# Kernel tuning notes

Measured on AMD Instinct MI355X. Metric: run time of the kernel, lower is better.

## Reference

```python
import jax, jax.numpy as jnp
import numpy as np

V, I, H, O = 10000, 64, 128, 128   # vocab, in_size, hidden_size, out_size
T, L = 4096, 64                    # num traces, max trace length


def setup_inputs() -> dict:
    key = jax.random.key(0)
    ks = jax.random.split(key, 18)
    s = 0.05
    n = jax.random.normal
    inp = {
        "emb":   n(ks[0], (V, I)) * s,
        # torch nn.LSTM layer 0: weight_ih [4H, I], weight_hh [4H, H], biases [4H]
        "W_ih1": n(ks[1], (4 * H, I)) * s,
        "W_hh1": n(ks[2], (4 * H, H)) * s,
        "b_ih1": n(ks[3], (4 * H,)) * s,
        "b_hh1": n(ks[4], (4 * H,)) * s,
        # layer 1
        "W_ih2": n(ks[5], (4 * H, H)) * s,
        "W_hh2": n(ks[6], (4 * H, H)) * s,
        "b_ih2": n(ks[7], (4 * H,)) * s,
        "b_hh2": n(ks[8], (4 * H,)) * s,
        # attention MLP: hidden -> 64 -> 1
        "Wp1":   n(ks[9], (64, H)) * s,
        "bp1":   n(ks[10], (64,)) * s,
        "Wp2":   n(ks[11], (1, 64)) * s,
        "bp2":   n(ks[12], (1,)) * s,
        # out_layer
        "W_out": n(ks[13], (O, H)) * s,
        "b_out": n(ks[14], (O,)) * s,
        "traces": jax.random.randint(ks[15], (T, L), 0, V, dtype=jnp.int32),
        "lengths": jnp.maximum(jax.random.randint(ks[16], (T,), 1, L + 1, dtype=jnp.int32), 1),
    }
    return inp


def _lstm_step(x, W_ih, b_ih, b_hh):
    # Single LSTM timestep from zero state (h0=c0=0), per token.
    # Gate order in torch: i, f, g, o. f*c0 = 0 so f is computed-but-unused.
    g = x @ W_ih.T + b_ih + b_hh                      # [T, L, 4H]
    i, f, c_hat, o = jnp.split(g, 4, axis=-1)
    c = jax.nn.sigmoid(i) * jnp.tanh(c_hat)
    return jax.nn.sigmoid(o) * jnp.tanh(c)            # [T, L, H]


def reference(emb, W_ih1, W_hh1, b_ih1, b_hh1, W_ih2, W_hh2, b_ih2, b_hh2,
              Wp1, bp1, Wp2, bp2, W_out, b_out, traces, lengths):
    x = emb[traces]                                   # [T, L, I]
    h1 = _lstm_step(x, W_ih1, b_ih1, b_hh1)           # [T, L, H]
    h2 = _lstm_step(h1, W_ih2, b_ih2, b_hh2)          # [T, L, H]  (hidden_out)
    # SelfAttention over positions within each trace
    energy = (jax.nn.relu(h2 @ Wp1.T + bp1) @ Wp2.T + bp2)[..., 0]  # [T, L]
    mask = jnp.arange(L)[None, :] < lengths[:, None]  # [T, L] valid positions
    energy = jnp.where(mask, energy, -1e30)
    w = jax.nn.softmax(energy, axis=1)                # [T, L]
    trace_emb = jnp.einsum("tlh,tl->th", h2, w)      # [T, H]
    final = trace_emb.sum(axis=0)                     # [H]  (sum over traces)
    return final @ W_out.T + b_out                    # [O]
```

## Files before the change

### kernel.cpp

```cpp
#include <hip/hip_runtime.h>
#include <stdint.h>

typedef unsigned short u16;
typedef __attribute__((ext_vector_type(8))) short short8;
typedef __attribute__((ext_vector_type(4))) float f32x4;
typedef __attribute__((ext_vector_type(4))) unsigned int u32x4;

#define NTRACE 4096
#define TLEN   64
#define ISZ    64
#define HSZ    128
#define NBIN   64
#define VSZ    10000

#define LOG2E     1.44269504088896f
#define TWOLOG2E  2.88539008177793f

__device__ __forceinline__ float bflo(uint32_t u) {
  union { uint32_t i; float f; } v; v.i = u << 16; return v.f;
}
__device__ __forceinline__ float bfhi(uint32_t u) {
  union { uint32_t i; float f; } v; v.i = u & 0xffff0000u; return v.f;
}
__device__ __forceinline__ u16 f2bf(float f) {
  union { float f; uint32_t i; } v; v.f = f;
  uint32_t r = v.i + 0x7fffu + ((v.i >> 16) & 1u);
  return (u16)(r >> 16);
}
__device__ __forceinline__ float fexp2(float x) {
  float r;
  asm("v_exp_f32 %0, %1" : "=v"(r) : "v"(x));
  return r;
}
__device__ __forceinline__ float gate2(float gB, float gE) {
  float E = fexp2(gE);
  float B = fexp2(gB);
  return (E - 1.0f) * __builtin_amdgcn_rcpf((E + 1.0f) * (1.0f + B));
}
__device__ __forceinline__ short8 mk8(uint32_t a, uint32_t b, uint32_t c, uint32_t d) {
  union { short8 s; uint32_t u[4]; } z;
  z.u[0] = a; z.u[1] = b; z.u[2] = c; z.u[3] = d; return z.s;
}
union S8 { short8 s; u16 h[8]; };
__device__ __forceinline__ int perm128(int rr) {
  return ((rr >> 4) & 3) * 32 + ((rr >> 2) & 3) * 8 + ((rr >> 6) & 1) * 4 + (rr & 3);
}

__global__ __launch_bounds__(256) void k_prep(
    const float* __restrict__ W1, const float* __restrict__ W2,
    const float* __restrict__ Wp1,
    const float* __restrict__ b_ih1, const float* __restrict__ b_hh1,
    const float* __restrict__ b_ih2, const float* __restrict__ b_hh2,
    u16* __restrict__ w1c, u16* __restrict__ w2c, u16* __restrict__ wp1b,
    float* __restrict__ bs1, float* __restrict__ bs2,
    float* __restrict__ bins)
{
  const int i = blockIdx.x * 256 + threadIdx.x;
  if (i < 3072) {
    const int r    = i >> 3;
    const int G3   = r >> 7;
    const int rawG = (G3 == 0) ? 0 : ((G3 == 1) ? 2 : 3);
    const int src  = rawG * 128 + perm128(r & 127);
    const float s  = (G3 == 1) ? TWOLOG2E : -LOG2E;
    const int c16  = (i & 7) * 8;
    const float* wsrc = W1 + (size_t)src * ISZ + c16;
    uint32_t pkk[4];
#pragma unroll
    for (int k = 0; k < 4; ++k)
      pkk[k] = (uint32_t)f2bf(wsrc[2 * k] * s) |
               ((uint32_t)f2bf(wsrc[2 * k + 1] * s) << 16);
    *(u32x4*)&w1c[r * 64 + (c16 ^ ((r & 7) << 3))] = *(u32x4*)pkk;
  }
  if (i < 6144) {
    const int r    = i >> 4;
    const int G3   = r >> 7;
    const int rawG = (G3 == 0) ? 0 : ((G3 == 1) ? 2 : 3);
    const int src  = rawG * 128 + perm128(r & 127);
    const float s  = (G3 == 1) ? TWOLOG2E : -LOG2E;
    const int c16  = (i & 15) * 8;
    const float* wsrc = W2 + (size_t)src * HSZ + c16;
    uint32_t pkk[4];
#pragma unroll
    for (int k = 0; k < 4; ++k)
      pkk[k] = (uint32_t)f2bf(wsrc[2 * k] * s) |
               ((uint32_t)f2bf(wsrc[2 * k + 1] * s) << 16);
    *(u32x4*)&w2c[r * 128 + (c16 ^ ((r & 15) << 3))] = *(u32x4*)pkk;
  }
  if (i < 64 * 128) wp1b[i] = f2bf(Wp1[i]);
  if (i < 512) {
    const int G = i >> 7, rr = i & 127;
    const float s = (G == 2) ? TWOLOG2E : -LOG2E;
    const int src = G * 128 + perm128(rr);
    bs1[i] = (b_ih1[src] + b_hh1[src]) * s;
    bs2[i] = (b_ih2[src] + b_hh2[src]) * s;
  }
  if (i < NBIN * HSZ) bins[i] = 0.f;
}

__global__ __launch_bounds__(512) void k_vocab(
    const float* __restrict__ emb,
    const u16* __restrict__ w1c, const u16* __restrict__ w2c,
    const float* __restrict__ bs1, const float* __restrict__ bs2,
    const u16* __restrict__ wp1b,
    const float* __restrict__ bp1v, const float* __restrict__ wp2v,
    float* __restrict__ Et, u16* __restrict__ H2t)
{
  __shared__ __align__(16) u16 w1s[384 * 64];
  __shared__ __align__(16) u16 w2s[384 * 128];
  const int tid = threadIdx.x;

  for (int i = tid; i < 3072; i += 512)
    ((u32x4*)w1s)[i] = ((const u32x4*)w1c)[i];
  for (int i = tid; i < 6144; i += 512)
    ((u32x4*)w2s)[i] = ((const u32x4*)w2c)[i];
  __syncthreads();

  const int lane = tid & 63;
  const int col  = lane & 15;
  const int q    = lane >> 4;
  const int sw1  = (col & 7) << 3;
  const int sw2  = col << 3;
  const int id   = (blockIdx.x * 8 + (tid >> 6)) * 16 + col;
  const int idc  = (id < VSZ) ? id : 0;
  const f32x4 z = {0.f, 0.f, 0.f, 0.f};

  short8 xf[2];
  {
    const float* xr = emb + (size_t)idc * ISZ + q * 8;
#pragma unroll
    for (int ks = 0; ks < 2; ++ks) {
      S8 v;
#pragma unroll
      for (int k = 0; k < 8; ++k) v.h[k] = f2bf(xr[ks * 32 + k]);
      xf[ks] = v.s;
    }
  }

  uint32_t pk[8][2];
#pragma unroll
  for (int mt = 0; mt < 8; ++mt) {
    f32x4 aI = z, aC = z, aO = z;
#pragma unroll
    for (int ks = 0; ks < 2; ++ks) {
      const int off = ((ks * 32 + q * 8) ^ sw1);
      short8 fI = *(const short8*)&w1s[(mt * 16 + col) * ISZ + off];
      short8 fC = *(const short8*)&w1s[(128 + mt * 16 + col) * ISZ + off];
      short8 fO = *(const short8*)&w1s[(256 + mt * 16 + col) * ISZ + off];
      aI = __builtin_amdgcn_mfma_f32_16x16x32_bf16(fI, xf[ks], aI, 0, 0, 0);
      aC = __builtin_amdgcn_mfma_f32_16x16x32_bf16(fC, xf[ks], aC, 0, 0, 0);
      aO = __builtin_amdgcn_mfma_f32_16x16x32_bf16(fO, xf[ks], aO, 0, 0, 0);
    }
    u16 hv[4];
#pragma unroll
    for (int r = 0; r < 4; ++r) {
      const int h = mt * 16 + q * 4 + r;
      float c = gate2(aI[r] + bs1[h], aC[r] + bs1[256 + h]);
      hv[r] = f2bf(gate2(aO[r] + bs1[384 + h], TWOLOG2E * c));
    }
    pk[mt][0] = (uint32_t)hv[0] | ((uint32_t)hv[1] << 16);
    pk[mt][1] = (uint32_t)hv[2] | ((uint32_t)hv[3] << 16);
  }

  short8 hf[4];
#pragma unroll
  for (int ks = 0; ks < 4; ++ks)
    hf[ks] = mk8(pk[ks][0], pk[ks][1], pk[ks + 4][0], pk[ks + 4][1]);

  uint32_t pk2[8][2];
#pragma unroll
  for (int mt = 0; mt < 8; ++mt) {
    f32x4 aI = z, aC = z, aO = z;
#pragma unroll
    for (int ks = 0; ks < 4; ++ks) {
      const int off = ((ks * 32 + q * 8) ^ sw2);
      short8 fI = *(const short8*)&w2s[(mt * 16 + col) * HSZ + off];
      short8 fC = *(const short8*)&w2s[(128 + mt * 16 + col) * HSZ + off];
      short8 fO = *(const short8*)&w2s[(256 + mt * 16 + col) * HSZ + off];
      aI = __builtin_amdgcn_mfma_f32_16x16x32_bf16(fI, hf[ks], aI, 0, 0, 0);
      aC = __builtin_amdgcn_mfma_f32_16x16x32_bf16(fC, hf[ks], aC, 0, 0, 0);
      aO = __builtin_amdgcn_mfma_f32_16x16x32_bf16(fO, hf[ks], aO, 0, 0, 0);
    }
    u16 hv[4];
#pragma unroll
    for (int r = 0; r < 4; ++r) {
      const int h = mt * 16 + q * 4 + r;
      float c = gate2(aI[r] + bs2[h], aC[r] + bs2[256 + h]);
      hv[r] = f2bf(gate2(aO[r] + bs2[384 + h], TWOLOG2E * c));
    }
    pk2[mt][0] = (uint32_t)hv[0] | ((uint32_t)hv[1] << 16);
    pk2[mt][1] = (uint32_t)hv[2] | ((uint32_t)hv[3] << 16);
  }

  short8 hf2[4];
#pragma unroll
  for (int ks = 0; ks < 4; ++ks)
    hf2[ks] = mk8(pk2[ks][0], pk2[ks][1], pk2[ks + 4][0], pk2[ks + 4][1]);

  float ep = 0.f;
#pragma unroll
  for (int mt = 0; mt < 4; ++mt) {
    f32x4 acc = z;
#pragma unroll
    for (int ks = 0; ks < 4; ++ks) {
      short8 fA = *(const short8*)(wp1b + (size_t)(mt * 16 + col) * HSZ + ks * 32 + q * 8);
      acc = __builtin_amdgcn_mfma_f32_16x16x32_bf16(fA, hf2[ks], acc, 0, 0, 0);
    }
#pragma unroll
    for (int r = 0; r < 4; ++r) {
      const int hp = mt * 16 + q * 4 + r;
      ep += fmaxf(acc[r] + bp1v[hp], 0.f) * wp2v[hp];
    }
  }
  ep += __shfl_xor(ep, 16);
  ep += __shfl_xor(ep, 32);

  if (id < VSZ) {
    if (q == 0) Et[id] = ep;
#pragma unroll
    for (int ks = 0; ks < 4; ++ks)
      *(short8*)&H2t[(size_t)id * HSZ + ks * 32 + q * 8] = hf2[ks];
  }
}

__global__ __launch_bounds__(256) void k_attn(
    const float* __restrict__ Et, const u16* __restrict__ H2t,
    const int* __restrict__ traces, const int* __restrict__ lengths,
    float* __restrict__ bins)
{
  const int wv   = threadIdx.x >> 6;
  const int lane = threadIdx.x & 63;
  const int t    = blockIdx.x * 4 + wv;
  const int len  = lengths[t];
  const int tok  = traces[t * TLEN + lane];
  const bool valid = lane < len;

  float e = valid ? Et[tok] : -3.0e38f;
  float m = e;
#pragma unroll
  for (int off = 1; off < 64; off <<= 1) m = fmaxf(m, __shfl_xor(m, off));
  float w = valid ? __expf(e - m) : 0.f;
  float s = w;
#pragma unroll
  for (int off = 1; off < 64; off <<= 1) s += __shfl_xor(s, off);
  const float wl = w * __builtin_amdgcn_rcpf(s);

  const int hc = lane * 2;
  float a0 = 0.f, a1 = 0.f;
  for (int l = 0; l < len; ++l) {
    const float wb = __shfl(wl, l);
    const int   tb = __shfl(tok, l);
    const uint32_t hv = *(const uint32_t*)&H2t[(size_t)tb * HSZ + hc];
    a0 += wb * bflo(hv);
    a1 += wb * bfhi(hv);
  }
  float* bin = bins + (size_t)(t & (NBIN - 1)) * HSZ;
  atomicAdd(&bin[hc], a0);
  atomicAdd(&bin[hc + 1], a1);
}

__global__ __launch_bounds__(128) void k_out(
    const float* __restrict__ bins, const float* __restrict__ W_out,
    const float* __restrict__ b_out, float* __restrict__ out)
{
  const int o = threadIdx.x;
  __shared__ float fs[HSZ];
  float s = 0.f;
#pragma unroll 4
  for (int b = 0; b < NBIN; ++b) s += bins[b * HSZ + o];
  fs[o] = s;
  __syncthreads();
  float acc = b_out[o];
  const float* wr = W_out + (size_t)o * HSZ;
#pragma unroll
  for (int h = 0; h < HSZ; ++h) acc += wr[h] * fs[h];
  out[o] = acc;
}

extern "C" void kernel_launch(void* const* d_in, const int* in_sizes, int n_in,
                              void* d_out, int out_size, void* d_ws, size_t ws_size,
                              hipStream_t stream)
{
  const float* emb   = (const float*)d_in[0];
  const float* W_ih1 = (const float*)d_in[1];
  const float* b_ih1 = (const float*)d_in[3];
  const float* b_hh1 = (const float*)d_in[4];
  const float* W_ih2 = (const float*)d_in[5];
  const float* b_ih2 = (const float*)d_in[7];
  const float* b_hh2 = (const float*)d_in[8];
  const float* Wp1   = (const float*)d_in[9];
  const float* bp1   = (const float*)d_in[10];
  const float* Wp2   = (const float*)d_in[11];
  const float* bp2   = (const float*)d_in[12];
  const float* W_out = (const float*)d_in[13];
  const float* b_out = (const float*)d_in[14];
  const int* traces  = (const int*)d_in[15];
  const int* lengths = (const int*)d_in[16];
  (void)bp2;

  char* ws = (char*)d_ws;
  float* Et   = (float*)(ws);
  u16*   H2t  = (u16*)(ws + 40960);
  float* bins = (float*)(ws + 2662400);
  u16*   w1c  = (u16*)(ws + 2695168);
  u16*   w2c  = (u16*)(ws + 2744320);
  u16*   wp1b = (u16*)(ws + 2842624);
  float* bs1  = (float*)(ws + 2859008);
  float* bs2  = (float*)(ws + 2861056);

  k_prep<<<32, 256, 0, stream>>>(W_ih1, W_ih2, Wp1, b_ih1, b_hh1,
                                 b_ih2, b_hh2, w1c, w2c, wp1b,
                                 bs1, bs2, bins);
  k_vocab<<<80, 512, 0, stream>>>(emb, w1c, w2c, bs1, bs2, wp1b,
                                  bp1, Wp2, Et, H2t);
  k_attn<<<NTRACE / 4, 256, 0, stream>>>(Et, H2t, traces, lengths, bins);
  k_out<<<1, 128, 0, stream>>>(bins, W_out, b_out, (float*)d_out);
}
```

Before: 138.3 us.

## Fuse weight prep into vocab kernel and output GEMV into attention kernel

Each of the 80 vocab blocks now converts the fp32 LSTM weights and biases to bf16 directly into shared memory, and converts Wp1 inline, so the separate prep kernel is gone. The output projection is folded into the attention kernel: an atomic counter picks the last block, which sums the bins and runs the output GEMV. This cuts the launch count from four to two, removing launch gaps and a workspace round trip. In exchange every vocab block repeats the fp32-to-bf16 conversion, and the attention kernel gains a threadfence, an atomic counter and atomic reads of the bins.

Result: slower. 152.6 us (+10.3%).

```diff
diff --git a/kernel.cpp b/kernel.cpp
--- a/kernel.cpp
+++ b/kernel.cpp
@@ -12,6 +12,7 @@
 #define HSZ    128
 #define NBIN   64
 #define VSZ    10000
+#define NATT   (NTRACE / 4)
 
 #define LOG2E     1.44269504088896f
 #define TWOLOG2E  2.88539008177793f
@@ -46,17 +47,29 @@
   return ((rr >> 4) & 3) * 32 + ((rr >> 2) & 3) * 8 + ((rr >> 6) & 1) * 4 + (rr & 3);
 }
 
-__global__ __launch_bounds__(256) void k_prep(
+__global__ __launch_bounds__(512) void k_vocab(
+    const float* __restrict__ emb,
     const float* __restrict__ W1, const float* __restrict__ W2,
-    const float* __restrict__ Wp1,
     const float* __restrict__ b_ih1, const float* __restrict__ b_hh1,
     const float* __restrict__ b_ih2, const float* __restrict__ b_hh2,
-    u16* __restrict__ w1c, u16* __restrict__ w2c, u16* __restrict__ wp1b,
-    float* __restrict__ bs1, float* __restrict__ bs2,
-    float* __restrict__ bins)
+    const float* __restrict__ Wp1,
+    const float* __restrict__ bp1v, const float* __restrict__ wp2v,
+    float* __restrict__ Et, u16* __restrict__ H2t,
+    float* __restrict__ bins, unsigned* __restrict__ ctr)
 {
-  const int i = blockIdx.x * 256 + threadIdx.x;
-  if (i < 3072) {
+  __shared__ __align__(16) u16 w1s[384 * 64];
+  __shared__ __align__(16) u16 w2s[384 * 128];
+  __shared__ float bsh1[512];
+  __shared__ float bsh2[512];
+  const int tid = threadIdx.x;
+
+  {
+    const int bz = blockIdx.x * 512 + tid;
+    if (bz < NBIN * HSZ) bins[bz] = 0.f;
+    if (blockIdx.x == 0 && tid == 0) *ctr = 0u;
+  }
+
+  for (int i = tid; i < 3072; i += 512) {
     const int r    = i >> 3;
     const int G3   = r >> 7;
     const int rawG = (G3 == 0) ? 0 : ((G3 == 1) ? 2 : 3);
@@ -69,9 +82,9 @@
     for (int k = 0; k < 4; ++k)
       pkk[k] = (uint32_t)f2bf(wsrc[2 * k] * s) |
                ((uint32_t)f2bf(wsrc[2 * k + 1] * s) << 16);
-    *(u32x4*)&w1c[r * 64 + (c16 ^ ((r & 7) << 3))] = *(u32x4*)pkk;
-  }
-  if (i < 6144) {
+    *(u32x4*)&w1s[r * 64 + (c16 ^ ((r & 7) << 3))] = *(u32x4*)pkk;
+  }
+  for (int i = tid; i < 6144; i += 512) {
     const int r    = i >> 4;
     const int G3   = r >> 7;
     const int rawG = (G3 == 0) ? 0 : ((G3 == 1) ? 2 : 3);
@@ -84,35 +97,15 @@
     for (int k = 0; k < 4; ++k)
       pkk[k] = (uint32_t)f2bf(wsrc[2 * k] * s) |
                ((uint32_t)f2bf(wsrc[2 * k + 1] * s) << 16);
-    *(u32x4*)&w2c[r * 128 + (c16 ^ ((r & 15) << 3))] = *(u32x4*)pkk;
-  }
-  if (i < 64 * 128) wp1b[i] = f2bf(Wp1[i]);
-  if (i < 512) {
-    const int G = i >> 7, rr = i & 127;
+    *(u32x4*)&w2s[r * 128 + (c16 ^ ((r & 15) << 3))] = *(u32x4*)pkk;
+  }
+  if (tid < 512) {
+    const int G = tid >> 7, rr = tid & 127;
     const float s = (G == 2) ? TWOLOG2E : -LOG2E;
     const int src = G * 128 + perm128(rr);
-    bs1[i] = (b_ih1[src] + b_hh1[src]) * s;
-    bs2[i] = (b_ih2[src] + b_hh2[src]) * s;
-  }
-  if (i < NBIN * HSZ) bins[i] = 0.f;
-}
-
-__global__ __launch_bounds__(512) void k_vocab(
-    const float* __restrict__ emb,
-    const u16* __restrict__ w1c, const u16* __restrict__ w2c,
-    const float* __restrict__ bs1, const float* __restrict__ bs2,
-    const u16* __restrict__ wp1b,
-    const float* __restrict__ bp1v, const float* __restrict__ wp2v,
-    float* __restrict__ Et, u16* __restrict__ H2t)
-{
-  __shared__ __align__(16) u16 w1s[384 * 64];
-  __shared__ __align__(16) u16 w2s[384 * 128];
-  const int tid = threadIdx.x;
-
-  for (int i = tid; i < 3072; i += 512)
-    ((u32x4*)w1s)[i] = ((const u32x4*)w1c)[i];
-  for (int i = tid; i < 6144; i += 512)
-    ((u32x4*)w2s)[i] = ((const u32x4*)w2c)[i];
+    bsh1[tid] = (b_ih1[src] + b_hh1[src]) * s;
+    bsh2[tid] = (b_ih2[src] + b_hh2[src]) * s;
+  }
   __syncthreads();
 
   const int lane = tid & 63;
@@ -154,8 +147,8 @@
 #pragma unroll
     for (int r = 0; r < 4; ++r) {
       const int h = mt * 16 + q * 4 + r;
-      float c = gate2(aI[r] + bs1[h], aC[r] + bs1[256 + h]);
-      hv[r] = f2bf(gate2(aO[r] + bs1[384 + h], TWOLOG2E * c));
+      float c = gate2(aI[r] + bsh1[h], aC[r] + bsh1[256 + h]);
+      hv[r] = f2bf(gate2(aO[r] + bsh1[384 + h], TWOLOG2E * c));
     }
     pk[mt][0] = (uint32_t)hv[0] | ((uint32_t)hv[1] << 16);
     pk[mt][1] = (uint32_t)hv[2] | ((uint32_t)hv[3] << 16);
@@ -184,8 +177,8 @@
 #pragma unroll
     for (int r = 0; r < 4; ++r) {
       const int h = mt * 16 + q * 4 + r;
-      float c = gate2(aI[r] + bs2[h], aC[r] + bs2[256 + h]);
-      hv[r] = f2bf(gate2(aO[r] + bs2[384 + h], TWOLOG2E * c));
+      float c = gate2(aI[r] + bsh2[h], aC[r] + bsh2[256 + h]);
+      hv[r] = f2bf(gate2(aO[r] + bsh2[384 + h], TWOLOG2E * c));
     }
     pk2[mt][0] = (uint32_t)hv[0] | ((uint32_t)hv[1] << 16);
     pk2[mt][1] = (uint32_t)hv[2] | ((uint32_t)hv[3] << 16);
@@ -202,8 +195,11 @@
     f32x4 acc = z;
 #pragma unroll
     for (int ks = 0; ks < 4; ++ks) {
-      short8 fA = *(const short8*)(wp1b + (size_t)(mt * 16 + col) * HSZ + ks * 32 + q * 8);
-      acc = __builtin_amdgcn_mfma_f32_16x16x32_bf16(fA, hf2[ks], acc, 0, 0, 0);
+      const float* wr = Wp1 + (size_t)(mt * 16 + col) * HSZ + ks * 32 + q * 8;
+      S8 v;
+#pragma unroll
+      for (int k = 0; k < 8; ++k) v.h[k] = f2bf(wr[k]);
+      acc = __builtin_amdgcn_mfma_f32_16x16x32_bf16(v.s, hf2[ks], acc, 0, 0, 0);
     }
 #pragma unroll
     for (int r = 0; r < 4; ++r) {
@@ -222,11 +218,15 @@
   }
 }
 
-__global__ __launch_bounds__(256) void k_attn(
+__global__ __launch_bounds__(256) void k_attn_out(
     const float* __restrict__ Et, const u16* __restrict__ H2t,
     const int* __restrict__ traces, const int* __restrict__ lengths,
-    float* __restrict__ bins)
+    float* __restrict__ bins, unsigned* __restrict__ ctr,
+    const float* __restrict__ W_out, const float* __restrict__ b_out,
+    float* __restrict__ out)
 {
+  __shared__ float fs[HSZ];
+  __shared__ int lastflag;
   const int wv   = threadIdx.x >> 6;
   const int lane = threadIdx.x & 63;
   const int t    = blockIdx.x * 4 + wv;
@@ -256,24 +256,35 @@
   float* bin = bins + (size_t)(t & (NBIN - 1)) * HSZ;
   atomicAdd(&bin[hc], a0);
   atomicAdd(&bin[hc + 1], a1);
-}
-
-__global__ __launch_bounds__(128) void k_out(
-    const float* __restrict__ bins, const float* __restrict__ W_out,
-    const float* __restrict__ b_out, float* __restrict__ out)
-{
-  const int o = threadIdx.x;
-  __shared__ float fs[HSZ];
-  float s = 0.f;
+
+  __syncthreads();
+  if (threadIdx.x == 0) {
+    __threadfence();
+    lastflag = (atomicAdd(ctr, 1u) == (unsigned)(NATT - 1)) ? 1 : 0;
+  }
+  __syncthreads();
+  if (lastflag) {
+    const int o = threadIdx.x;
+    if (o < HSZ) {
+      float acc = 0.f;
 #pragma unroll 4
-  for (int b = 0; b < NBIN; ++b) s += bins[b * HSZ + o];
-  fs[o] = s;
-  __syncthreads();
-  float acc = b_out[o];
-  const float* wr = W_out + (size_t)o * HSZ;
-#pragma unroll
-  for (int h = 0; h < HSZ; ++h) acc += wr[h] * fs[h];
-  out[o] = acc;
+      for (int b = 0; b < NBIN; ++b)
+        acc += atomicAdd(&bins[(size_t)b * HSZ + o], 0.f);
+      fs[o] = acc;
+    }
+    __syncthreads();
+    if (o < HSZ) {
+      float acc = b_out[o];
+      const float* wr = W_out + (size_t)o * HSZ;
+#pragma unroll 8
+      for (int h = 0; h < HSZ; h += 4) {
+        const f32x4 wv4 = *(const f32x4*)&wr[h];
+        acc += wv4[0] * fs[h] + wv4[1] * fs[h + 1]
+             + wv4[2] * fs[h + 2] + wv4[3] * fs[h + 3];
+      }
+      out[o] = acc;
+    }
+  }
 }
 
 extern "C" void kernel_launch(void* const* d_in, const int* in_sizes, int n_in,
@@ -298,20 +309,15 @@
   (void)bp2;
 
   char* ws = (char*)d_ws;
-  float* Et   = (float*)(ws);
-  u16*   H2t  = (u16*)(ws + 40960);
-  float* bins = (float*)(ws + 2662400);
-  u16*   w1c  = (u16*)(ws + 2695168);
-  u16*   w2c  = (u16*)(ws + 2744320);
-  u16*   wp1b = (u16*)(ws + 2842624);
-  float* bs1  = (float*)(ws + 2859008);
-  float* bs2  = (float*)(ws + 2861056);
-
-  k_prep<<<32, 256, 0, stream>>>(W_ih1, W_ih2, Wp1, b_ih1, b_hh1,
-                                 b_ih2, b_hh2, w1c, w2c, wp1b,
-                                 bs1, bs2, bins);
-  k_vocab<<<80, 512, 0, stream>>>(emb, w1c, w2c, bs1, bs2, wp1b,
-                                  bp1, Wp2, Et, H2t);
-  k_attn<<<NTRACE / 4, 256, 0, stream>>>(Et, H2t, traces, lengths, bins);
-  k_out<<<1, 128, 0, stream>>>(bins, W_out, b_out, (float*)d_out);
-}
+  float*    Et   = (float*)(ws);
+  u16*      H2t  = (u16*)(ws + 40960);
+  float*    bins = (float*)(ws + 2662400);
+  unsigned* ctr  = (unsigned*)(ws + 2695168);
+
+  k_vocab<<<80, 512, 0, stream>>>(emb, W_ih1, W_ih2, b_ih1, b_hh1,
+                                  b_ih2, b_hh2, Wp1, bp1, Wp2,
+                                  Et, H2t, bins, ctr);
+  k_attn_out<<<NATT, 256, 0, stream>>>(Et, H2t, traces, lengths,
+                                       bins, ctr, W_out, b_out,
+                                       (float*)d_out);
+}
```
